# Kernel optimization log

Measured on AMD Instinct MI355X. Metric: run time of the kernel, lower is better.

## Reference

```python
import jax, jax.numpy as jnp
import numpy as np

B, N_DISKS, D_MODEL, N_HEADS = 64, 253, 1024, 16


def setup_inputs() -> dict:
    key = jax.random.key(0)
    ks = jax.random.split(key, 9)
    S = N_DISKS + 3
    scale = 1.0 / np.sqrt(D_MODEL)
    x = jax.random.normal(ks[0], (B, S, D_MODEL), jnp.float32)
    state = jax.random.randint(ks[1], (B, N_DISKS), 0, 3)
    padding_mask = jnp.ones((B, N_DISKS), dtype=bool)
    W_Q = jax.random.normal(ks[2], (D_MODEL, D_MODEL), jnp.float32) * scale
    W_K = jax.random.normal(ks[3], (D_MODEL, D_MODEL), jnp.float32) * scale
    W_V = jax.random.normal(ks[4], (D_MODEL, D_MODEL), jnp.float32) * scale
    W_O = jax.random.normal(ks[5], (D_MODEL, D_MODEL), jnp.float32) * scale
    b_O = jnp.zeros((D_MODEL,), jnp.float32)
    edge_type_bias = jax.random.normal(ks[6], (4,), jnp.float32) * 0.1
    same_rod_bias = jax.random.normal(ks[7], (2,), jnp.float32) * 0.1
    relative_size_bias = jax.random.normal(ks[8], (3,), jnp.float32) * 0.1
    return dict(x=x, state=state, padding_mask=padding_mask, W_Q=W_Q, W_K=W_K,
                W_V=W_V, W_O=W_O, b_O=b_O, edge_type_bias=edge_type_bias,
                same_rod_bias=same_rod_bias, relative_size_bias=relative_size_bias,
                N=N_DISKS, n_heads=N_HEADS)


def _structural_bias(state, edge_type_bias, same_rod_bias, relative_size_bias, S):
    # Vectorized equivalent of the original triple Python loop.
    idx = jnp.arange(S)
    is_disk = idx >= 3
    # edge type: (disk,disk)->0, (disk,rod)->1, (rod,disk)->2, (rod,rod)->3
    ei = 2 * (~is_disk[:, None]).astype(jnp.int32) + (~is_disk[None, :]).astype(jnp.int32)
    bias = edge_type_bias[ei]  # (S, S)
    Bsz = state.shape[0]
    bias = jnp.broadcast_to(bias, (Bsz, S, S))
    # same-rod bias (disk-disk only)
    same = state[:, :, None] == state[:, None, :]  # (B, N, N)
    rod_b = jnp.where(same, same_rod_bias[0], same_rod_bias[1])
    # relative size bias (disk-disk; i==j case is excluded by the diagonal skip)
    di = idx[3:]
    size_b = jnp.where(di[:, None] < di[None, :], relative_size_bias[0], relative_size_bias[2])
    bias = bias.at[:, 3:, 3:].add(rod_b + size_b)
    # original code skips i == j entirely
    diag = jnp.eye(S, dtype=bool)
    return jnp.where(diag[None, :, :], 0.0, bias)


def reference(x, state, padding_mask, W_Q, W_K, W_V, W_O, b_O,
              edge_type_bias, same_rod_bias, relative_size_bias, N, n_heads):
    Bsz, S, d = x.shape
    d_k = d // n_heads
    # LayerNorm (no affine), eps = 1e-5 like F.layer_norm default
    mu = jnp.mean(x, axis=-1, keepdims=True)
    var = jnp.mean((x - mu) ** 2, axis=-1, keepdims=True)
    xn = (x - mu) / jnp.sqrt(var + 1e-5)

    def proj(W):  # torch Linear: y = x @ W.T
        return jnp.einsum('bsd,ed->bse', xn, W).reshape(Bsz, S, n_heads, d_k).transpose(0, 2, 1, 3)

    Q, K, V = proj(W_Q), proj(W_K), proj(W_V)
    scores = jnp.einsum('bhqd,bhkd->bhqk', Q, K) / jnp.sqrt(jnp.float32(d_k))
    bias = _structural_bias(state, edge_type_bias, same_rod_bias, relative_size_bias, S)
    scores = scores + bias[:, None, :, :]
    full_mask = jnp.concatenate([jnp.ones((Bsz, 3), dtype=bool), padding_mask], axis=1)
    m = full_mask[:, None, None, :] & full_mask[:, None, :, None]
    scores = jnp.where(m, scores, -jnp.inf)
    attn = jax.nn.softmax(scores, axis=-1)
    attn = jnp.nan_to_num(attn, nan=0.0)
    out = jnp.einsum('bhqk,bhkd->bhqd', attn, V).transpose(0, 2, 1, 3).reshape(Bsz, S, d)
    out = jnp.einsum('bsd,ed->bse', out, W_O) + b_O
    return x + out
```

## Files before the change

### kernel.cpp

```cpp
#include <hip/hip_runtime.h>
#include <hip/hip_bf16.h>
#include <stdint.h>

typedef float f32x4_t __attribute__((ext_vector_type(4)));
typedef short bf16x8_t __attribute__((ext_vector_type(8)));

#define MFMA16(a, b, c) __builtin_amdgcn_mfma_f32_16x16x32_bf16((a), (b), (c), 0, 0, 0)

static __device__ __forceinline__ unsigned short f2bf(float f) {
  union { float f; unsigned int u; } v;
  v.f = f;
  unsigned int u = v.u;
  unsigned int r = (u + 0x7fffu + ((u >> 16) & 1u)) >> 16;
  return (unsigned short)r;
}

static __device__ __forceinline__ void gll16(const unsigned short* g, unsigned short* l) {
  __builtin_amdgcn_global_load_lds(
      (const __attribute__((address_space(1))) unsigned int*)g,
      (__attribute__((address_space(3))) unsigned int*)l, 16, 0, 0);
}

__global__ __launch_bounds__(256) void cvt4_kernel(const float* __restrict__ s0,
                                                   const float* __restrict__ s1,
                                                   const float* __restrict__ s2,
                                                   const float* __restrict__ s3,
                                                   unsigned short* __restrict__ dst) {
  const int i = blockIdx.x * 256 + threadIdx.x;
  const float* src = (blockIdx.y == 0) ? s0 : (blockIdx.y == 1) ? s1 : (blockIdx.y == 2) ? s2 : s3;
  float4 v = ((const float4*)src)[i];
  ushort4 o;
  o.x = f2bf(v.x); o.y = f2bf(v.y); o.z = f2bf(v.z); o.w = f2bf(v.w);
  ((ushort4*)(dst + (size_t)blockIdx.y * 1048576))[i] = o;
}

__global__ __launch_bounds__(256) void ln_kernel(const float* __restrict__ x,
                                                 unsigned short* __restrict__ xn) {
  const int row = blockIdx.x;
  const int tid = threadIdx.x, w = tid >> 6, lane = tid & 63;
  const float4 v = ((const float4*)(x + (size_t)row * 1024))[tid];
  float s = v.x + v.y + v.z + v.w;
  float s2 = v.x * v.x + v.y * v.y + v.z * v.z + v.w * v.w;
#pragma unroll
  for (int m = 32; m; m >>= 1) {
    s += __shfl_xor(s, m, 64);
    s2 += __shfl_xor(s2, m, 64);
  }
  __shared__ float red[2][4];
  if (lane == 0) { red[0][w] = s; red[1][w] = s2; }
  __syncthreads();
  const float S = red[0][0] + red[0][1] + red[0][2] + red[0][3];
  const float S2 = red[1][0] + red[1][1] + red[1][2] + red[1][3];
  const float mu = S * (1.0f / 1024.0f);
  const float var = S2 * (1.0f / 1024.0f) - mu * mu;
  const float rstd = rsqrtf(var + 1e-5f);
  ushort4 o;
  o.x = f2bf((v.x - mu) * rstd);
  o.y = f2bf((v.y - mu) * rstd);
  o.z = f2bf((v.z - mu) * rstd);
  o.w = f2bf((v.w - mu) * rstd);
  ((ushort4*)(xn + (size_t)row * 1024))[tid] = o;
}

template <int MODE>
__global__ __launch_bounds__(512, 1) void gemm_pipe(
    const unsigned short* __restrict__ A, const unsigned short* __restrict__ B,
    unsigned short* __restrict__ Qo, unsigned short* __restrict__ Ko,
    unsigned short* __restrict__ Vo, float* __restrict__ Cf,
    const float* __restrict__ bias, const float* __restrict__ resid, int GX) {
  constexpr int K = 1024;
  constexpr int NT = 16;
  __shared__ __align__(16) unsigned short lds[73728];
  const int tid = threadIdx.x;
  const int wv = tid >> 6, lane = tid & 63;
  const int l15 = lane & 15, l4 = lane >> 4;
  const int wr = wv >> 1, wc = wv & 1;
  const int fid = blockIdx.y * GX + blockIdx.x;
  const int cpx = (GX * gridDim.y) >> 3;
  const int swz = (fid & 7) * cpx + (fid >> 3);
  const int bm = swz / GX, bn = swz % GX;

  const int srow = wv * 8 + (lane >> 3);
  const int schunk = ((lane & 7) ^ (lane >> 3)) * 8;
  const unsigned short* Ag = A + (size_t)(bm * 256 + srow) * K + schunk;
  const unsigned short* Bg = B + (size_t)(bn * 128 + srow) * K + schunk;

  f32x4_t acc[4][4];
#pragma unroll
  for (int i = 0; i < 4; ++i)
#pragma unroll
    for (int j = 0; j < 4; ++j) acc[i][j] = (f32x4_t){0.f, 0.f, 0.f, 0.f};

#define STAGE(tt, slot)                                                          \
  {                                                                              \
    const unsigned short* As_ = Ag + (tt)*64;                                    \
    const unsigned short* Bs_ = Bg + (tt)*64;                                    \
    _Pragma("unroll") for (int r = 0; r < 4; ++r)                                \
        gll16(As_ + (size_t)(r * 64) * K, &lds[(slot)*16384 + r * 4096 + wv * 512]); \
    _Pragma("unroll") for (int r = 0; r < 2; ++r)                                \
        gll16(Bs_ + (size_t)(r * 64) * K,                                        \
              &lds[49152 + (slot)*8192 + r * 4096 + wv * 512]);                  \
  }

#define CONSUME(slot)                                                            \
  {                                                                              \
    const unsigned short* As_ = &lds[(slot)*16384];                              \
    const unsigned short* Bs_ = &lds[49152 + (slot)*8192];                       \
    _Pragma("unroll") for (int kk = 0; kk < 2; ++kk) {                           \
      const int cx = 8 * (((kk * 4 + l4) ^ (l15 & 7)));                          \
      bf16x8_t af[4], bf[4];                                                     \
      _Pragma("unroll") for (int m = 0; m < 4; ++m)                              \
          af[m] = *(const bf16x8_t*)&As_[(wr * 64 + m * 16 + l15) * 64 + cx];    \
      _Pragma("unroll") for (int n = 0; n < 4; ++n)                              \
          bf[n] = *(const bf16x8_t*)&Bs_[(wc * 64 + n * 16 + l15) * 64 + cx];    \
      __builtin_amdgcn_s_setprio(1);                                             \
      _Pragma("unroll") for (int m = 0; m < 4; ++m)                              \
          _Pragma("unroll") for (int n = 0; n < 4; ++n)                          \
              acc[m][n] = MFMA16(af[m], bf[n], acc[m][n]);                       \
      __builtin_amdgcn_s_setprio(0);                                             \
    }                                                                            \
  }

  STAGE(0, 0);
  STAGE(1, 1);
  asm volatile("s_waitcnt vmcnt(6)" ::: "memory");
  __builtin_amdgcn_s_barrier();
  asm volatile("" ::: "memory");

#pragma unroll 1
  for (int t = 0; t < NT - 2; ++t) {
    const int s = t % 3;
    const int sp = (t + 2) % 3;
    STAGE(t + 2, sp);
    CONSUME(s);
    asm volatile("s_waitcnt vmcnt(6)" ::: "memory");
    __builtin_amdgcn_s_barrier();
    asm volatile("" ::: "memory");
  }
  CONSUME((NT - 2) % 3);
  asm volatile("s_waitcnt vmcnt(0)" ::: "memory");
  __builtin_amdgcn_s_barrier();
  asm volatile("" ::: "memory");
  CONSUME((NT - 1) % 3);

#undef STAGE
#undef CONSUME

  const int rbase = bm * 256 + wr * 64;
  const int cbase = bn * 128 + wc * 64;
  if constexpr (MODE == 3) {
    if (bn < 16) {
      unsigned short* Out = (bn < 8) ? Qo : Ko;
      const int coff = (bn < 8) ? 0 : 1024;
#pragma unroll
      for (int i = 0; i < 4; ++i) {
        const int row0 = rbase + i * 16 + l4 * 4;
#pragma unroll
        for (int j = 0; j < 4; ++j) {
          const int col = cbase + j * 16 + l15 - coff;
#pragma unroll
          for (int r = 0; r < 4; ++r) Out[(size_t)(row0 + r) * 1024 + col] = f2bf(acc[i][j][r]);
        }
      }
    } else {
#pragma unroll
      for (int i = 0; i < 4; ++i) {
        const int row0 = rbase + i * 16 + l4 * 4;
        const int bb = row0 >> 8, s0 = row0 & 255;
#pragma unroll
        for (int j = 0; j < 4; ++j) {
          const int e = cbase + j * 16 + l15 - 2048;
          const int d = e & 63;
          const int sr = (s0 + d * 8) & 255;
          ushort4 pk;
          pk.x = f2bf(acc[i][j][0]); pk.y = f2bf(acc[i][j][1]);
          pk.z = f2bf(acc[i][j][2]); pk.w = f2bf(acc[i][j][3]);
          *(ushort4*)&Vo[((size_t)bb * 1024 + e) * 256 + sr] = pk;
        }
      }
    }
  } else {
#pragma unroll
    for (int i = 0; i < 4; ++i) {
      const int row0 = rbase + i * 16 + l4 * 4;
#pragma unroll
      for (int j = 0; j < 4; ++j) {
        const int col = cbase + j * 16 + l15;
        const float bo = bias[col];
#pragma unroll
        for (int r = 0; r < 4; ++r) {
          const size_t idx = (size_t)(row0 + r) * 1024 + col;
          Cf[idx] = acc[i][j][r] + bo + resid[idx];
        }
      }
    }
  }
}

__global__ __launch_bounds__(256, 4) void attn_kernel(
    const unsigned short* __restrict__ Q, const unsigned short* __restrict__ K,
    const unsigned short* __restrict__ Vt, unsigned short* __restrict__ O,
    const int* __restrict__ state, const float* __restrict__ etb,
    const float* __restrict__ srb, const float* __restrict__ rsb) {
  const int cp = blockIdx.x, h = blockIdx.y, b = blockIdx.z;
  const int tid = threadIdx.x, w = tid >> 6, lane = tid & 63;
  const int l15 = lane & 15, l4 = lane >> 4;

  __shared__ __align__(16) unsigned short Vs[64 * 256];
  __shared__ __align__(16) unsigned short Ps[4][16 * 136];
  __shared__ int state_s[256];

  const unsigned short* Vg = Vt + ((size_t)b * 1024 + h * 64) * 256;
#pragma unroll
  for (int rnd = 0; rnd < 8; ++rnd) {
    const int ob = (rnd * 4 + w) * 512;
    gll16(Vg + ob + lane * 8, &Vs[ob]);
  }
  state_s[tid] = (tid >= 3) ? state[b * 253 + tid - 3] : 0x7fffffff;
  const float e0 = etb[0], e1 = etb[1], e2 = etb[2], e3 = etb[3];
  const float sr0 = srb[0], sr1 = srb[1];
  const float rs0 = rsb[0], rs2 = rsb[2];
  __syncthreads();

#pragma unroll
  for (int c = 0; c < 2; ++c) {
    const int qrow0 = cp * 128 + w * 32 + c * 16;
    const size_t qoff = (size_t)(b * 256 + qrow0 + l15) * 1024 + h * 64 + l4 * 8;
    const bf16x8_t qf0 = *(const bf16x8_t*)(Q + qoff);
    const bf16x8_t qf1 = *(const bf16x8_t*)(Q + qoff + 32);

    const int qr0 = qrow0 + l4 * 4;
    int sq[4];
#pragma unroll
    for (int r = 0; r < 4; ++r) sq[r] = state_s[qr0 + r];

    f32x4_t oacc[4];
#pragma unroll
    for (int n = 0; n < 4; ++n) oacc[n] = (f32x4_t){0.f, 0.f, 0.f, 0.f};
    float rsum[4] = {0.f, 0.f, 0.f, 0.f};

#pragma unroll
    for (int half = 0; half < 2; ++half) {
      f32x4_t sc[8];
#pragma unroll
      for (int f = 0; f < 8; ++f) sc[f] = (f32x4_t){0.f, 0.f, 0.f, 0.f};
      const unsigned short* Kb2 =
          K + (size_t)(b * 256 + half * 128) * 1024 + h * 64 + l4 * 8;
#pragma unroll
      for (int f = 0; f < 8; ++f) {
        const unsigned short* kp = Kb2 + (size_t)(f * 16 + l15) * 1024;
        sc[f] = MFMA16(qf0, *(const bf16x8_t*)kp, sc[f]);
        sc[f] = MFMA16(qf1, *(const bf16x8_t*)(kp + 32), sc[f]);
      }

#pragma unroll
      for (int f = 0; f < 8; ++f) {
        const int kcol = half * 128 + f * 16 + l15;
        const bool kd = kcol >= 3;
        const int skc = state_s[kcol];
#pragma unroll
        for (int r = 0; r < 4; ++r) {
          const int qrow = qr0 + r;
          float bd = e0 + ((skc == sq[r]) ? sr0 : sr1) + ((qrow < kcol) ? rs0 : rs2);
          float bv = (qrow >= 3) ? (kd ? bd : e1) : (kd ? e2 : e3);
          bv = (qrow == kcol) ? 0.f : bv;
          const float p = __expf(fmaf(sc[f][r], 0.125f, bv));
          rsum[r] += p;
          Ps[w][(l4 * 4 + r) * 136 + f * 16 + l15] = f2bf(p);
        }
      }

#pragma unroll
      for (int kbl = 0; kbl < 4; ++kbl) {
        const bf16x8_t pf = *(const bf16x8_t*)&Ps[w][l15 * 136 + kbl * 32 + l4 * 8];
        const int kb = half * 4 + kbl;
#pragma unroll
        for (int n = 0; n < 4; ++n) {
          const int d = n * 16 + l15;
          const int scol = (kb * 32 + l4 * 8 + d * 8) & 255;
          const bf16x8_t vf = *(const bf16x8_t*)&Vs[d * 256 + scol];
          oacc[n] = MFMA16(pf, vf, oacc[n]);
        }
      }
    }

#pragma unroll
    for (int m = 1; m < 16; m <<= 1)
#pragma unroll
      for (int r = 0; r < 4; ++r) rsum[r] += __shfl_xor(rsum[r], m, 64);
    float rinv[4];
#pragma unroll
    for (int r = 0; r < 4; ++r) rinv[r] = 1.0f / rsum[r];
    unsigned short* Op = O + (size_t)(b * 256 + qr0) * 1024 + h * 64;
#pragma unroll
    for (int n = 0; n < 4; ++n)
#pragma unroll
      for (int r = 0; r < 4; ++r)
        Op[(size_t)r * 1024 + n * 16 + l15] = f2bf(oacc[n][r] * rinv[r]);
  }
}

extern "C" void kernel_launch(void* const* d_in, const int* in_sizes, int n_in,
                              void* d_out, int out_size, void* d_ws, size_t ws_size,
                              hipStream_t stream) {
  const float* x = (const float*)d_in[0];
  const int* state = (const int*)d_in[1];
  const float* WQ = (const float*)d_in[3];
  const float* WK = (const float*)d_in[4];
  const float* WV = (const float*)d_in[5];
  const float* WO = (const float*)d_in[6];
  const float* bO = (const float*)d_in[7];
  const float* etb = (const float*)d_in[8];
  const float* srb = (const float*)d_in[9];
  const float* rsb = (const float*)d_in[10];

  char* ws = (char*)d_ws;
  unsigned short* xn = (unsigned short*)(ws);
  unsigned short* Vt = (unsigned short*)(ws + (size_t)(32 << 20));
  unsigned short* WQKVb = (unsigned short*)(ws + (size_t)(64 << 20));
  unsigned short* WOb = WQKVb + (3 << 20);
  unsigned short* Qb = (unsigned short*)d_out;
  unsigned short* Kb = Qb + (16 << 20);

  cvt4_kernel<<<dim3(1024, 4), 256, 0, stream>>>(WQ, WK, WV, WO, WQKVb);
  ln_kernel<<<16384, 256, 0, stream>>>(x, xn);

  gemm_pipe<3><<<dim3(24, 64), 512, 0, stream>>>(xn, WQKVb, Qb, Kb, Vt, nullptr,
                                                 nullptr, nullptr, 24);

  attn_kernel<<<dim3(2, 16, 64), 256, 0, stream>>>(Qb, Kb, Vt, xn, state, etb, srb, rsb);

  gemm_pipe<2><<<dim3(8, 64), 512, 0, stream>>>(xn, WOb, nullptr, nullptr, nullptr,
                                                (float*)d_out, bO, x, 8);
}
```

Measured before the change: 273.3 us.

## Give each attention wave its own head and query tile, reading V from global

The attention kernel is restructured so each wave handles one (head, 16-row query tile) pair, with each block's four waves spanning different heads, instead of a block staging one head's full V into LDS. V fragments now come straight from global memory, so the V GEMM epilogue writes V-transposed without the swizzle, and the big LDS buffer is removed. The softmax exponent uses exp2f with log2(e) folded into the scale and the biases. This should raise occupancy and remove the LDS staging cost, but it gives up V reuse across waves and relies on L2 for the repeated V reads.

```diff
diff --git a/kernel.cpp b/kernel.cpp
--- a/kernel.cpp
+++ b/kernel.cpp
@@ -170,12 +170,10 @@
 #pragma unroll
         for (int j = 0; j < 4; ++j) {
           const int e = cbase + j * 16 + l15 - 2048;
-          const int d = e & 63;
-          const int sr = (s0 + d * 8) & 255;
           ushort4 pk;
           pk.x = f2bf(acc[i][j][0]); pk.y = f2bf(acc[i][j][1]);
           pk.z = f2bf(acc[i][j][2]); pk.w = f2bf(acc[i][j][3]);
-          *(ushort4*)&Vo[((size_t)bb * 1024 + e) * 256 + sr] = pk;
+          *(ushort4*)&Vo[((size_t)bb * 1024 + e) * 256 + s0] = pk;
         }
       }
     }
@@ -202,102 +200,95 @@
     const unsigned short* __restrict__ Vt, unsigned short* __restrict__ O,
     const int* __restrict__ state, const float* __restrict__ etb,
     const float* __restrict__ srb, const float* __restrict__ rsb) {
-  const int cp = blockIdx.x, h = blockIdx.y, b = blockIdx.z;
+  const int b = blockIdx.y;
   const int tid = threadIdx.x, w = tid >> 6, lane = tid & 63;
   const int l15 = lane & 15, l4 = lane >> 4;
-
-  __shared__ __align__(16) unsigned short Vs[64 * 256];
+  const int id = blockIdx.x * 4 + w;
+  const int h = id & 15;
+  const int qrow0 = (id >> 4) * 16;
+
   __shared__ __align__(16) unsigned short Ps[4][16 * 136];
   __shared__ int state_s[256];
 
-  const unsigned short* Vg = Vt + ((size_t)b * 1024 + h * 64) * 256;
-#pragma unroll
-  for (int rnd = 0; rnd < 8; ++rnd) {
-    const int ob = (rnd * 4 + w) * 512;
-    gll16(Vg + ob + lane * 8, &Vs[ob]);
-  }
   state_s[tid] = (tid >= 3) ? state[b * 253 + tid - 3] : 0x7fffffff;
-  const float e0 = etb[0], e1 = etb[1], e2 = etb[2], e3 = etb[3];
-  const float sr0 = srb[0], sr1 = srb[1];
-  const float rs0 = rsb[0], rs2 = rsb[2];
+  constexpr float L2E = 1.4426950408889634f;
+  const float e0 = etb[0] * L2E, e1 = etb[1] * L2E, e2 = etb[2] * L2E, e3 = etb[3] * L2E;
+  const float sr0 = srb[0] * L2E, sr1 = srb[1] * L2E;
+  const float rs0 = rsb[0] * L2E, rs2 = rsb[2] * L2E;
   __syncthreads();
 
-#pragma unroll
-  for (int c = 0; c < 2; ++c) {
-    const int qrow0 = cp * 128 + w * 32 + c * 16;
-    const size_t qoff = (size_t)(b * 256 + qrow0 + l15) * 1024 + h * 64 + l4 * 8;
-    const bf16x8_t qf0 = *(const bf16x8_t*)(Q + qoff);
-    const bf16x8_t qf1 = *(const bf16x8_t*)(Q + qoff + 32);
-
-    const int qr0 = qrow0 + l4 * 4;
-    int sq[4];
-#pragma unroll
-    for (int r = 0; r < 4; ++r) sq[r] = state_s[qr0 + r];
-
-    f32x4_t oacc[4];
-#pragma unroll
-    for (int n = 0; n < 4; ++n) oacc[n] = (f32x4_t){0.f, 0.f, 0.f, 0.f};
-    float rsum[4] = {0.f, 0.f, 0.f, 0.f};
-
-#pragma unroll
-    for (int half = 0; half < 2; ++half) {
-      f32x4_t sc[8];
-#pragma unroll
-      for (int f = 0; f < 8; ++f) sc[f] = (f32x4_t){0.f, 0.f, 0.f, 0.f};
-      const unsigned short* Kb2 =
-          K + (size_t)(b * 256 + half * 128) * 1024 + h * 64 + l4 * 8;
-#pragma unroll
-      for (int f = 0; f < 8; ++f) {
-        const unsigned short* kp = Kb2 + (size_t)(f * 16 + l15) * 1024;
-        sc[f] = MFMA16(qf0, *(const bf16x8_t*)kp, sc[f]);
-        sc[f] = MFMA16(qf1, *(const bf16x8_t*)(kp + 32), sc[f]);
-      }
-
-#pragma unroll
-      for (int f = 0; f < 8; ++f) {
-        const int kcol = half * 128 + f * 16 + l15;
-        const bool kd = kcol >= 3;
-        const int skc = state_s[kcol];
-#pragma unroll
-        for (int r = 0; r < 4; ++r) {
-          const int qrow = qr0 + r;
-          float bd = e0 + ((skc == sq[r]) ? sr0 : sr1) + ((qrow < kcol) ? rs0 : rs2);
-          float bv = (qrow >= 3) ? (kd ? bd : e1) : (kd ? e2 : e3);
-          bv = (qrow == kcol) ? 0.f : bv;
-          const float p = __expf(fmaf(sc[f][r], 0.125f, bv));
-          rsum[r] += p;
-          Ps[w][(l4 * 4 + r) * 136 + f * 16 + l15] = f2bf(p);
-        }
-      }
-
-#pragma unroll
-      for (int kbl = 0; kbl < 4; ++kbl) {
-        const bf16x8_t pf = *(const bf16x8_t*)&Ps[w][l15 * 136 + kbl * 32 + l4 * 8];
-        const int kb = half * 4 + kbl;
-#pragma unroll
-        for (int n = 0; n < 4; ++n) {
-          const int d = n * 16 + l15;
-          const int scol = (kb * 32 + l4 * 8 + d * 8) & 255;
-          const bf16x8_t vf = *(const bf16x8_t*)&Vs[d * 256 + scol];
-          oacc[n] = MFMA16(pf, vf, oacc[n]);
-        }
-      }
-    }
-
-#pragma unroll
-    for (int m = 1; m < 16; m <<= 1)
-#pragma unroll
-      for (int r = 0; r < 4; ++r) rsum[r] += __shfl_xor(rsum[r], m, 64);
-    float rinv[4];
-#pragma unroll
-    for (int r = 0; r < 4; ++r) rinv[r] = 1.0f / rsum[r];
-    unsigned short* Op = O + (size_t)(b * 256 + qr0) * 1024 + h * 64;
-#pragma unroll
-    for (int n = 0; n < 4; ++n)
-#pragma unroll
-      for (int r = 0; r < 4; ++r)
-        Op[(size_t)r * 1024 + n * 16 + l15] = f2bf(oacc[n][r] * rinv[r]);
-  }
+  const size_t qoff = (size_t)(b * 256 + qrow0 + l15) * 1024 + h * 64 + l4 * 8;
+  const bf16x8_t qf0 = *(const bf16x8_t*)(Q + qoff);
+  const bf16x8_t qf1 = *(const bf16x8_t*)(Q + qoff + 32);
+
+  const int qr0 = qrow0 + l4 * 4;
+  int sq[4];
+#pragma unroll
+  for (int r = 0; r < 4; ++r) sq[r] = state_s[qr0 + r];
+
+  f32x4_t oacc[4];
+#pragma unroll
+  for (int n = 0; n < 4; ++n) oacc[n] = (f32x4_t){0.f, 0.f, 0.f, 0.f};
+  float rsum[4] = {0.f, 0.f, 0.f, 0.f};
+  const unsigned short* Vb = Vt + ((size_t)b * 1024 + h * 64) * 256;
+
+#pragma unroll
+  for (int half = 0; half < 2; ++half) {
+    f32x4_t sc[8];
+#pragma unroll
+    for (int f = 0; f < 8; ++f) sc[f] = (f32x4_t){0.f, 0.f, 0.f, 0.f};
+    const unsigned short* Kb2 =
+        K + (size_t)(b * 256 + half * 128) * 1024 + h * 64 + l4 * 8;
+#pragma unroll
+    for (int f = 0; f < 8; ++f) {
+      const unsigned short* kp = Kb2 + (size_t)(f * 16 + l15) * 1024;
+      sc[f] = MFMA16(qf0, *(const bf16x8_t*)kp, sc[f]);
+      sc[f] = MFMA16(qf1, *(const bf16x8_t*)(kp + 32), sc[f]);
+    }
+
+#pragma unroll
+    for (int f = 0; f < 8; ++f) {
+      const int kcol = half * 128 + f * 16 + l15;
+      const bool kd = kcol >= 3;
+      const int skc = state_s[kcol];
+#pragma unroll
+      for (int r = 0; r < 4; ++r) {
+        const int qrow = qr0 + r;
+        float bd = e0 + ((skc == sq[r]) ? sr0 : sr1) + ((qrow < kcol) ? rs0 : rs2);
+        float bv = (qrow >= 3) ? (kd ? bd : e1) : (kd ? e2 : e3);
+        bv = (qrow == kcol) ? 0.f : bv;
+        const float p = exp2f(fmaf(sc[f][r], 0.18033688011112042f, bv));
+        rsum[r] += p;
+        Ps[w][(l4 * 4 + r) * 136 + f * 16 + l15] = f2bf(p);
+      }
+    }
+
+#pragma unroll
+    for (int kbl = 0; kbl < 4; ++kbl) {
+      const bf16x8_t pf = *(const bf16x8_t*)&Ps[w][l15 * 136 + kbl * 32 + l4 * 8];
+      const int kb = half * 4 + kbl;
+#pragma unroll
+      for (int n = 0; n < 4; ++n) {
+        const int d = n * 16 + l15;
+        const bf16x8_t vf = *(const bf16x8_t*)(Vb + (size_t)d * 256 + kb * 32 + l4 * 8);
+        oacc[n] = MFMA16(pf, vf, oacc[n]);
+      }
+    }
+  }
+
+#pragma unroll
+  for (int m = 1; m < 16; m <<= 1)
+#pragma unroll
+    for (int r = 0; r < 4; ++r) rsum[r] += __shfl_xor(rsum[r], m, 64);
+  float rinv[4];
+#pragma unroll
+  for (int r = 0; r < 4; ++r) rinv[r] = 1.0f / rsum[r];
+  unsigned short* Op = O + (size_t)(b * 256 + qr0) * 1024 + h * 64;
+#pragma unroll
+  for (int n = 0; n < 4; ++n)
+#pragma unroll
+    for (int r = 0; r < 4; ++r)
+      Op[(size_t)r * 1024 + n * 16 + l15] = f2bf(oacc[n][r] * rinv[r]);
 }
 
 extern "C" void kernel_launch(void* const* d_in, const int* in_sizes, int n_in,
@@ -328,7 +319,7 @@
   gemm_pipe<3><<<dim3(24, 64), 512, 0, stream>>>(xn, WQKVb, Qb, Kb, Vt, nullptr,
                                                  nullptr, nullptr, 24);
 
-  attn_kernel<<<dim3(2, 16, 64), 256, 0, stream>>>(Qb, Kb, Vt, xn, state, etb, srb, rsb);
+  attn_kernel<<<dim3(64, 64), 256, 0, stream>>>(Qb, Kb, Vt, xn, state, etb, srb, rsb);
 
   gemm_pipe<2><<<dim3(8, 64), 512, 0, stream>>>(xn, WOb, nullptr, nullptr, nullptr,
                                                 (float*)d_out, bO, x, 8);
```

New measurement: 322.3 us. +17.9%, slower.
